# Kernel tuning notes

Measured on AMD Instinct MI355X. Metric: run time of the kernel, lower is better.

The kernel has to match this reference:

```python
import jax, jax.numpy as jnp
import numpy as np

EMBED_DIM = 768
NUM_HEADS = 12
HEAD_DIM = EMBED_DIM // NUM_HEADS


def setup_inputs() -> dict:
    key = jax.random.key(0)
    k_x, k_qkv_w, k_qkv_b, k_pw, k_pb = jax.random.split(key, 5)
    B, S = 16, 1024
    scale = 1.0 / np.sqrt(EMBED_DIM)
    return {
        "x": jax.random.normal(k_x, (B, S, EMBED_DIM), dtype=jnp.float32),
        "qkv_w": jax.random.normal(k_qkv_w, (EMBED_DIM, 3 * EMBED_DIM), dtype=jnp.float32) * scale,
        "qkv_b": jax.random.normal(k_qkv_b, (3 * EMBED_DIM,), dtype=jnp.float32) * 0.02,
        "proj_w": jax.random.normal(k_pw, (EMBED_DIM, EMBED_DIM), dtype=jnp.float32) * scale,
        "proj_b": jax.random.normal(k_pb, (EMBED_DIM,), dtype=jnp.float32) * 0.02,
    }


def reference(x, qkv_w, qkv_b, proj_w, proj_b):
    B, S, E = x.shape
    H, D = NUM_HEADS, HEAD_DIM
    qkv = x @ qkv_w + qkv_b                      # [B, S, 3E]
    qkv = qkv.reshape(B, S, 3, H, D)
    qkv = jnp.transpose(qkv, (2, 0, 3, 1, 4))    # [3, B, H, S, D]
    q, k, v = qkv[0], qkv[1], qkv[2]
    scores = jnp.einsum("bhqd,bhkd->bhqk", q, k) / jnp.sqrt(jnp.float32(D))
    probs = jax.nn.softmax(scores, axis=-1)      # dropout is identity in eval
    attn = jnp.einsum("bhqk,bhkd->bhqd", probs, v)
    attn = jnp.transpose(attn, (0, 2, 1, 3)).reshape(B, S, E)
    return attn @ proj_w + proj_b
```

## Files before the change

### kernel.cpp

```cpp
#include <hip/hip_runtime.h>
#include <hip/hip_bf16.h>

typedef unsigned short u16;
typedef unsigned int u32;
typedef short s16x8 __attribute__((ext_vector_type(8)));
typedef float f32x4 __attribute__((ext_vector_type(4)));

#define EMB 768
#define NH 12
#define HD 64
#define BB 16
#define SS 1024
#define MTOK (BB*SS)
#define NQKV (3*EMB)
#define QSZ ((size_t)BB*NH*SS*HD)

#define GLOBAL_AS const __attribute__((address_space(1))) void*
#define LDS_AS __attribute__((address_space(3))) void*

#if __has_builtin(__builtin_amdgcn_exp2f)
#define EXP2(x) __builtin_amdgcn_exp2f(x)
#else
#define EXP2(x) exp2f(x)
#endif

__device__ __forceinline__ u16 f2bf(float f){
  unsigned u = __float_as_uint(f);
  u += 0x7FFFu + ((u >> 16) & 1u);
  return (u16)(u >> 16);
}
__device__ __forceinline__ u16 f2bf_trunc(float f){
  return (u16)(__float_as_uint(f) >> 16);
}
__device__ __forceinline__ f32x4 mfma16(s16x8 a, s16x8 b, f32x4 c){
  return __builtin_amdgcn_mfma_f32_16x16x32_bf16(a, b, c, 0, 0, 0);
}

#define NBA 12288
#define NBB 1728
#define NBC 576

__device__ __forceinline__ void transpose_body(
    u16 (*tile)[33], const float* __restrict__ in, u16* __restrict__ out,
    int R, int C, int bxi, int byi){
  int bx = bxi * 32, by = byi * 32;
  int tx = threadIdx.x & 31, ty = threadIdx.x >> 5;
  #pragma unroll
  for(int i = 0; i < 32; i += 8)
    tile[ty + i][tx] = f2bf(in[(size_t)(by + ty + i) * C + bx + tx]);
  __syncthreads();
  #pragma unroll
  for(int i = 0; i < 32; i += 8)
    out[(size_t)(bx + ty + i) * R + by + tx] = tile[tx][ty + i];
}

__global__ __launch_bounds__(256) void prep_kernel(
    const float4* __restrict__ x4, ushort4* __restrict__ xb4,
    const float* __restrict__ qkv_w, u16* __restrict__ qkv_wT,
    const float* __restrict__ proj_w, u16* __restrict__ proj_wT){
  __shared__ u16 tile[32][33];
  int bid = blockIdx.x;
  if(bid < NBA){
    int i = bid * 256 + threadIdx.x;
    float4 f = x4[i];
    ushort4 o;
    o.x = f2bf(f.x); o.y = f2bf(f.y); o.z = f2bf(f.z); o.w = f2bf(f.w);
    xb4[i] = o;
  } else if(bid < NBA + NBB){
    int bi = bid - NBA;
    transpose_body(tile, qkv_w, qkv_wT, EMB, NQKV, bi % (NQKV/32), bi / (NQKV/32));
  } else {
    int bi = bid - NBA - NBB;
    transpose_body(tile, proj_w, proj_wT, EMB, EMB, bi % (EMB/32), bi / (EMB/32));
  }
}

__global__ __launch_bounds__(256) void qkv_gemm_kernel(
    const u16* __restrict__ A, const u16* __restrict__ Bt,
    const float* __restrict__ bias,
    u16* __restrict__ Qo, u16* __restrict__ Ko, u16* __restrict__ Vo){
  const int K = 768;
  __shared__ u16 SH[4][128*64];
  u16 (*As)[128*64] = &SH[0];
  u16 (*Bs)[128*64] = &SH[2];
  int tid = threadIdx.x;

  int gx = gridDim.x;
  int nwg = gx * gridDim.y;
  int L = blockIdx.y * gx + blockIdx.x;
  int nl = (L & 7) * (nwg >> 3) + (L >> 3);
  int m0 = (nl / gx) * 128, n0 = (nl % gx) * 128;

  int w = tid >> 6, lane = tid & 63, quad = lane >> 4, l15 = lane & 15;
  int wm = (w >> 1) * 64, wn = (w & 1) * 64;
  int rr = lane >> 3;
  int cp = lane & 7;
  f32x4 acc[4][4] = {};

  auto stage = [&](int p, int k0){
    #pragma unroll
    for(int it = 0; it < 4; ++it){
      int ci = it * 4 + w;
      int r  = ci * 8 + rr;
      int gc = (cp ^ (r & 7)) * 8;
      __builtin_amdgcn_global_load_lds(
          (GLOBAL_AS)(A + (size_t)(m0 + r) * K + k0 + gc),
          (LDS_AS)(As[p] + ci * 512 + lane * 8), 16, 0, 0);
      __builtin_amdgcn_global_load_lds(
          (GLOBAL_AS)(Bt + (size_t)(n0 + r) * K + k0 + gc),
          (LDS_AS)(Bs[p] + ci * 512 + lane * 8), 16, 0, 0);
    }
  };

  stage(0, 0);
  int p = 0;
  for(int k0 = 0; k0 < K; k0 += 64){
    __syncthreads();
    if(k0 + 64 < K) stage(p ^ 1, k0 + 64);
    #pragma unroll
    for(int kk = 0; kk < 2; kk++){
      s16x8 a[4], b[4];
      int ch = ((kk * 4 + quad) ^ (l15 & 7)) * 8;
      #pragma unroll
      for(int i = 0; i < 4; i++){
        a[i] = *(const s16x8*)&As[p][(wm + i*16 + l15) * 64 + ch];
        b[i] = *(const s16x8*)&Bs[p][(wn + i*16 + l15) * 64 + ch];
      }
      #pragma unroll
      for(int mt = 0; mt < 4; mt++)
        #pragma unroll
        for(int nt = 0; nt < 4; nt++)
          acc[mt][nt] = mfma16(a[mt], b[nt], acc[mt][nt]);
    }
    p ^= 1;
  }

  int which = (n0 + wn) / EMB;
  if(which == 2){
    #pragma unroll
    for(int mt = 0; mt < 4; mt++){
      #pragma unroll
      for(int nt = 0; nt < 4; nt++){
        int n = n0 + wn + nt*16 + l15;
        float bv = bias[n];
        int rem = n - 2 * EMB;
        int h = rem >> 6, d = rem & 63;
        int mbase = m0 + wm + mt*16 + quad*4;
        int bb = mbase >> 10, sb = mbase & 1023;
        size_t bh = (size_t)(bb * NH + h);
        ushort4 pk;
        pk.x = f2bf(acc[mt][nt][0] + bv);
        pk.y = f2bf(acc[mt][nt][1] + bv);
        pk.z = f2bf(acc[mt][nt][2] + bv);
        pk.w = f2bf(acc[mt][nt][3] + bv);
        *(ushort4*)&Vo[(bh * HD + d) * SS + sb] = pk;
      }
    }
  } else {
    u16* ep = &SH[0][0];
    __syncthreads();
    #pragma unroll
    for(int mt = 0; mt < 4; mt++){
      #pragma unroll
      for(int nt = 0; nt < 4; nt++){
        int n = n0 + wn + nt*16 + l15;
        float bv = bias[n];
        int row0 = wm + mt*16 + quad*4;
        #pragma unroll
        for(int r = 0; r < 4; r++)
          ep[(row0 + r) * 136 + wn + nt*16 + l15] = f2bf(acc[mt][nt][r] + bv);
      }
    }
    __syncthreads();
    u16* dst = (which == 0) ? Qo : Ko;
    int nb = n0 - which * EMB;
    #pragma unroll
    for(int pass = 0; pass < 8; ++pass){
      int c = pass * 256 + tid;
      int row = c >> 4, chunk = c & 15;
      s16x8 v = *(const s16x8*)&ep[row * 136 + chunk * 8];
      int m = m0 + row;
      int bb = m >> 10, ss = m & 1023;
      int rem = nb + chunk * 8;
      int h = rem >> 6, d = rem & 63;
      size_t bh = (size_t)(bb * NH + h);
      *(s16x8*)&dst[(bh * SS + ss) * HD + d] = v;
    }
  }
}

__global__ __launch_bounds__(512, 2) void proj_gemm_kernel(
    const u16* __restrict__ A, const u16* __restrict__ Bt,
    const float* __restrict__ bias, float* __restrict__ out){
  const int K = 768, NT = 12;
  __shared__ u16 As[2][256*64];
  __shared__ u16 Bs[2][256*64];
  int tid = threadIdx.x;

  int gx = gridDim.x;
  int nwg = gx * gridDim.y;
  int L = blockIdx.y * gx + blockIdx.x;
  int nl = (L & 7) * (nwg >> 3) + (L >> 3);
  int m0 = (nl / gx) * 256, n0 = (nl % gx) * 256;

  int w = tid >> 6, lane = tid & 63, quad = lane >> 4, l15 = lane & 15;
  int wm = (w >> 2) * 128, wn = (w & 3) * 64;
  int rr = lane >> 3;
  int cp = lane & 7;
  f32x4 acc[8][4] = {};

  auto stageQ = [&](int t, int q){
    int d = t & 1, k0 = t * 64;
    const u16* src = (q < 2) ? A : Bt;
    int base = (q < 2) ? m0 : n0;
    u16* dst = (q < 2) ? As[d] : Bs[d];
    int h = q & 1;
    #pragma unroll
    for(int it = 0; it < 2; ++it){
      int ci = h*16 + it*8 + w;
      int r  = ci * 8 + rr;
      int gc = (cp ^ (r & 7)) * 8;
      __builtin_amdgcn_global_load_lds(
          (GLOBAL_AS)(src + (size_t)(base + r) * K + k0 + gc),
          (LDS_AS)(dst + ci * 512 + lane * 8), 16, 0, 0);
    }
  };

  s16x8 a[8], b0[4], b1[4];
  auto dsA = [&](int d, int mh){
    #pragma unroll
    for(int kk = 0; kk < 2; ++kk){
      int ch = ((kk*4 + quad) ^ (l15 & 7)) * 8;
      #pragma unroll
      for(int i = 0; i < 4; ++i)
        a[kk*4+i] = *(const s16x8*)&As[d][(wm + (mh*4+i)*16 + l15) * 64 + ch];
    }
  };
  auto dsB = [&](int d, int nh, s16x8* bb){
    #pragma unroll
    for(int kk = 0; kk < 2; ++kk){
      int ch = ((kk*4 + quad) ^ (l15 & 7)) * 8;
      #pragma unroll
      for(int j = 0; j < 2; ++j)
        bb[kk*2+j] = *(const s16x8*)&Bs[d][(wn + (nh*2+j)*16 + l15) * 64 + ch];
    }
  };
  auto mfmaQ = [&](int mh, int nh, const s16x8* bb){
    __builtin_amdgcn_s_setprio(1);
    #pragma unroll
    for(int kk = 0; kk < 2; ++kk)
      #pragma unroll
      for(int i = 0; i < 4; ++i)
        #pragma unroll
        for(int j = 0; j < 2; ++j)
          acc[mh*4+i][nh*2+j] = mfma16(bb[kk*2+j], a[kk*4+i], acc[mh*4+i][nh*2+j]);
    __builtin_amdgcn_s_setprio(0);
  };

#define PHASE_SYNC() do{ \
    __builtin_amdgcn_s_barrier(); \
    asm volatile("s_waitcnt lgkmcnt(0)" ::: "memory"); \
    __builtin_amdgcn_sched_barrier(0); \
  }while(0)
#define PHASE_END() do{ \
    __builtin_amdgcn_s_barrier(); \
    __builtin_amdgcn_sched_barrier(0); \
  }while(0)

  stageQ(0,0); stageQ(0,1); stageQ(0,2); stageQ(0,3);
  stageQ(1,0);
  asm volatile("s_waitcnt vmcnt(2)" ::: "memory");
  __builtin_amdgcn_s_barrier();
  __builtin_amdgcn_sched_barrier(0);

  #pragma unroll
  for(int j = 0; j < NT/2; ++j){
    int t = 2*j;
    stageQ(t+1, 1);
    dsA(0, 0); dsB(0, 0, b0);
    PHASE_SYNC(); mfmaQ(0, 0, b0); PHASE_END();
    stageQ(t+1, 2);
    dsB(0, 1, b1);
    PHASE_SYNC(); mfmaQ(0, 1, b1); PHASE_END();
    stageQ(t+1, 3);
    dsA(0, 1);
    PHASE_SYNC(); mfmaQ(1, 0, b0); PHASE_END();
    if(t+2 < NT){ stageQ(t+2, 0); asm volatile("s_waitcnt vmcnt(2)" ::: "memory"); }
    else        { asm volatile("s_waitcnt vmcnt(0)" ::: "memory"); }
    PHASE_SYNC(); mfmaQ(1, 1, b1); PHASE_END();
    if(t+2 < NT) stageQ(t+2, 1);
    dsA(1, 0); dsB(1, 0, b0);
    PHASE_SYNC(); mfmaQ(0, 0, b0); PHASE_END();
    if(t+2 < NT) stageQ(t+2, 2);
    dsB(1, 1, b1);
    PHASE_SYNC(); mfmaQ(0, 1, b1); PHASE_END();
    if(t+2 < NT) stageQ(t+2, 3);
    dsA(1, 1);
    PHASE_SYNC(); mfmaQ(1, 0, b0); PHASE_END();
    if(t+3 < NT){ stageQ(t+3, 0); asm volatile("s_waitcnt vmcnt(2)" ::: "memory"); }
    else if(t+2 < NT){ asm volatile("s_waitcnt vmcnt(0)" ::: "memory"); }
    PHASE_SYNC(); mfmaQ(1, 1, b1); PHASE_END();
  }
#undef PHASE_SYNC
#undef PHASE_END

  #pragma unroll
  for(int mt = 0; mt < 8; ++mt){
    int m = m0 + wm + mt*16 + l15;
    #pragma unroll
    for(int nt = 0; nt < 4; ++nt){
      int nb = n0 + wn + nt*16 + quad*4;
      float4 bv = *(const float4*)&bias[nb];
      float4 v;
      v.x = acc[mt][nt][0] + bv.x;
      v.y = acc[mt][nt][1] + bv.y;
      v.z = acc[mt][nt][2] + bv.z;
      v.w = acc[mt][nt][3] + bv.w;
      *(float4*)&out[(size_t)m * EMB + nb] = v;
    }
  }
}

__global__ __launch_bounds__(512) void attn_kernel(
    const u16* __restrict__ Qws, const u16* __restrict__ Kws,
    const u16* __restrict__ Vtws, u16* __restrict__ attn){
  __shared__ u16 Ks[2][64*64];
  __shared__ u16 Vs[2][64*64];
  __shared__ __align__(16) u16 Ps[8][2][16][76];
  int tid = threadIdx.x;
  int w = tid >> 6, lane = tid & 63, quad = lane >> 4, l15 = lane & 15;
  int bh = blockIdx.x;
  int b = bh / NH, h = bh - b * NH;
  int q0 = blockIdx.y * 256 + w * 32;
  const u16* Qbase = Qws  + (size_t)bh * SS * HD;
  const u16* Kbase = Kws  + (size_t)bh * SS * HD;
  const u16* Vbase = Vtws + (size_t)bh * HD * SS;

  s16x8 aq[2][2];
  #pragma unroll
  for(int m = 0; m < 2; m++){
    int qrow = q0 + m*16 + l15;
    #pragma unroll
    for(int kk = 0; kk < 2; kk++)
      aq[m][kk] = *(const s16x8*)(Qbase + (size_t)qrow * HD + kk*32 + quad*8);
  }

  f32x4 o[2][4] = {};
  float psum[2][4] = {};
  const float C1 = 0.125f * 1.44269504f;
  const float C0 = -30.0f * 1.44269504f;

  int krr = lane >> 3, kcp = lane & 7;

  auto stageKV = [&](int p, int kt){
    int ins = w;
    int r   = ins * 8 + krr;
    int gck = (kcp ^ (r & 7)) * 8;
    __builtin_amdgcn_global_load_lds(
        (GLOBAL_AS)(Kbase + (size_t)(kt*64 + r) * HD + gck),
        (LDS_AS)(Ks[p] + ins * 512 + lane * 8), 16, 0, 0);
    __builtin_amdgcn_global_load_lds(
        (GLOBAL_AS)(Vbase + (size_t)r * SS + kt*64 + gck),
        (LDS_AS)(Vs[p] + ins * 512 + lane * 8), 16, 0, 0);
  };

  stageKV(0, 0);
  int p = 0;
  for(int kt = 0; kt < 16; ++kt){
    __syncthreads();
    if(kt < 15) stageKV(p ^ 1, kt + 1);

    #pragma unroll
    for(int nt = 0; nt < 4; ++nt){
      s16x8 bk[2];
      #pragma unroll
      for(int kk = 0; kk < 2; kk++){
        int ch = ((kk*4 + quad) ^ (l15 & 7)) * 8;
        bk[kk] = *(const s16x8*)&Ks[p][(nt*16 + l15) * 64 + ch];
      }
      #pragma unroll
      for(int m = 0; m < 2; m++){
        f32x4 z = {};
        z = mfma16(aq[m][0], bk[0], z);
        z = mfma16(aq[m][1], bk[1], z);
        #pragma unroll
        for(int r = 0; r < 4; r++){
          float pv = EXP2(z[r] * C1 + C0);
          psum[m][r] += pv;
          Ps[w][m][quad*4 + r][nt*16 + l15] = f2bf_trunc(pv);
        }
      }
    }
    #pragma unroll
    for(int k4 = 0; k4 < 2; k4++){
      s16x8 pa[2];
      #pragma unroll
      for(int m = 0; m < 2; m++)
        pa[m] = *(const s16x8*)&Ps[w][m][l15][k4*32 + quad*8];
      #pragma unroll
      for(int nt = 0; nt < 4; nt++){
        int ch = ((k4*4 + quad) ^ (l15 & 7)) * 8;
        s16x8 vb = *(const s16x8*)&Vs[p][(nt*16 + l15) * 64 + ch];
        #pragma unroll
        for(int m = 0; m < 2; m++)
          o[m][nt] = mfma16(pa[m], vb, o[m][nt]);
      }
    }
    p ^= 1;
  }

  #pragma unroll
  for(int m = 0; m < 2; m++){
    #pragma unroll
    for(int r = 0; r < 4; r++){
      float s = psum[m][r];
      s += __shfl_xor(s, 1, 64);
      s += __shfl_xor(s, 2, 64);
      s += __shfl_xor(s, 4, 64);
      s += __shfl_xor(s, 8, 64);
      float inv = 1.0f / s;
      int srow = q0 + m*16 + quad*4 + r;
      size_t base = ((size_t)(b * SS + srow)) * EMB + h * HD;
      #pragma unroll
      for(int nt = 0; nt < 4; nt++)
        attn[base + nt*16 + l15] = f2bf(o[m][nt][r] * inv);
    }
  }
}

extern "C" void kernel_launch(void* const* d_in, const int* in_sizes, int n_in,
                              void* d_out, int out_size, void* d_ws, size_t ws_size,
                              hipStream_t stream){
  const float* x      = (const float*)d_in[0];
  const float* qkv_w  = (const float*)d_in[1];
  const float* qkv_b  = (const float*)d_in[2];
  const float* proj_w = (const float*)d_in[3];
  const float* proj_b = (const float*)d_in[4];

  char* ws = (char*)d_ws;
  u16* qkv_wT  = (u16*)ws; ws += (size_t)NQKV * EMB * 2;
  u16* proj_wT = (u16*)ws; ws += (size_t)EMB * EMB * 2;
  u16* x_bf = (u16*)ws; ws += QSZ * 2;
  u16* Qws  = (u16*)ws; ws += QSZ * 2;
  u16* Kws  = (u16*)ws; ws += QSZ * 2;
  u16* Vtws = (u16*)ws; ws += QSZ * 2;
  u16* attn = x_bf;

  prep_kernel<<<NBA + NBB + NBC, 256, 0, stream>>>(
      (const float4*)x, (ushort4*)x_bf, qkv_w, qkv_wT, proj_w, proj_wT);
  qkv_gemm_kernel<<<dim3(NQKV/128, MTOK/128), 256, 0, stream>>>(
      x_bf, qkv_wT, qkv_b, Qws, Kws, Vtws);
  attn_kernel<<<dim3(BB*NH, SS/256), 512, 0, stream>>>(Qws, Kws, Vtws, attn);
  proj_gemm_kernel<<<dim3(EMB/256, MTOK/256), 512, 0, stream>>>(
      attn, proj_wT, proj_b, (float*)d_out);
}
```

Measured before the change: 277.2 us.

## Load V fragments directly from global into registers, drop V LDS staging

After: 601.2 us. 2.17x slower.

```diff
diff --git a/kernel.cpp b/kernel.cpp
--- a/kernel.cpp
+++ b/kernel.cpp
@@ -321,12 +321,11 @@
   }
 }
 
-__global__ __launch_bounds__(512) void attn_kernel(
+__global__ __launch_bounds__(512, 6) void attn_kernel(
     const u16* __restrict__ Qws, const u16* __restrict__ Kws,
     const u16* __restrict__ Vtws, u16* __restrict__ attn){
   __shared__ u16 Ks[2][64*64];
-  __shared__ u16 Vs[2][64*64];
-  __shared__ __align__(16) u16 Ps[8][2][16][76];
+  __shared__ __align__(16) u16 Ps[8][2][16][72];
   int tid = threadIdx.x;
   int w = tid >> 6, lane = tid & 63, quad = lane >> 4, l15 = lane & 15;
   int bh = blockIdx.x;
@@ -352,26 +351,28 @@
 
   int krr = lane >> 3, kcp = lane & 7;
 
-  auto stageKV = [&](int p, int kt){
-    int ins = w;
-    int r   = ins * 8 + krr;
+  auto stageK = [&](int p, int kt){
+    int r   = w * 8 + krr;
     int gck = (kcp ^ (r & 7)) * 8;
     __builtin_amdgcn_global_load_lds(
         (GLOBAL_AS)(Kbase + (size_t)(kt*64 + r) * HD + gck),
-        (LDS_AS)(Ks[p] + ins * 512 + lane * 8), 16, 0, 0);
-    __builtin_amdgcn_global_load_lds(
-        (GLOBAL_AS)(Vbase + (size_t)r * SS + kt*64 + gck),
-        (LDS_AS)(Vs[p] + ins * 512 + lane * 8), 16, 0, 0);
-  };
-
-  stageKV(0, 0);
+        (LDS_AS)(Ks[p] + w * 512 + lane * 8), 16, 0, 0);
+  };
+
+  stageK(0, 0);
   int p = 0;
   for(int kt = 0; kt < 16; ++kt){
     __syncthreads();
-    if(kt < 15) stageKV(p ^ 1, kt + 1);
-
-    #pragma unroll
-    for(int nt = 0; nt < 4; ++nt){
+
+    s16x8 va[4], vb[4];
+    #pragma unroll
+    for(int nt = 0; nt < 4; nt++)
+      va[nt] = *(const s16x8*)(Vbase + (size_t)(nt*16 + l15) * SS
+                               + kt*64 + quad*8);
+    if(kt < 15) stageK(p ^ 1, kt + 1);
+
+    #pragma unroll
+    for(int nt = 0; nt < 2; ++nt){
       s16x8 bk[2];
       #pragma unroll
       for(int kk = 0; kk < 2; kk++){
@@ -391,20 +392,52 @@
         }
       }
     }
-    #pragma unroll
-    for(int k4 = 0; k4 < 2; k4++){
+
+    #pragma unroll
+    for(int nt = 0; nt < 4; nt++)
+      vb[nt] = *(const s16x8*)(Vbase + (size_t)(nt*16 + l15) * SS
+                               + kt*64 + 32 + quad*8);
+
+    #pragma unroll
+    for(int nt = 2; nt < 4; ++nt){
+      s16x8 bk[2];
+      #pragma unroll
+      for(int kk = 0; kk < 2; kk++){
+        int ch = ((kk*4 + quad) ^ (l15 & 7)) * 8;
+        bk[kk] = *(const s16x8*)&Ks[p][(nt*16 + l15) * 64 + ch];
+      }
+      #pragma unroll
+      for(int m = 0; m < 2; m++){
+        f32x4 z = {};
+        z = mfma16(aq[m][0], bk[0], z);
+        z = mfma16(aq[m][1], bk[1], z);
+        #pragma unroll
+        for(int r = 0; r < 4; r++){
+          float pv = EXP2(z[r] * C1 + C0);
+          psum[m][r] += pv;
+          Ps[w][m][quad*4 + r][nt*16 + l15] = f2bf_trunc(pv);
+        }
+      }
+    }
+
+    {
       s16x8 pa[2];
       #pragma unroll
       for(int m = 0; m < 2; m++)
-        pa[m] = *(const s16x8*)&Ps[w][m][l15][k4*32 + quad*8];
-      #pragma unroll
-      for(int nt = 0; nt < 4; nt++){
-        int ch = ((k4*4 + quad) ^ (l15 & 7)) * 8;
-        s16x8 vb = *(const s16x8*)&Vs[p][(nt*16 + l15) * 64 + ch];
+        pa[m] = *(const s16x8*)&Ps[w][m][l15][quad*8];
+      #pragma unroll
+      for(int nt = 0; nt < 4; nt++)
         #pragma unroll
         for(int m = 0; m < 2; m++)
-          o[m][nt] = mfma16(pa[m], vb, o[m][nt]);
-      }
+          o[m][nt] = mfma16(pa[m], va[nt], o[m][nt]);
+      #pragma unroll
+      for(int m = 0; m < 2; m++)
+        pa[m] = *(const s16x8*)&Ps[w][m][l15][32 + quad*8];
+      #pragma unroll
+      for(int nt = 0; nt < 4; nt++)
+        #pragma unroll
+        for(int m = 0; m < 2; m++)
+          o[m][nt] = mfma16(pa[m], vb[nt], o[m][nt]);
     }
     p ^= 1;
   }
```
